# Optimization experiments

Hardware: AMD Instinct MI355X
Metric: run time of the kernel (lower is better)

## Reference

```python
import jax, jax.numpy as jnp
import numpy as np

B, S, D = 4, 1024, 1024
NS = 8            # n_samples
NT = 10           # n_steps
EXP_NOISE = 0.1
STEP = 0.01
TEMP = 1.0
LN_EPS = 1e-5


def _ln(x, g, b):
    m = jnp.mean(x, axis=-1, keepdims=True)
    v = jnp.mean(jnp.square(x - m), axis=-1, keepdims=True)
    return (x - m) * jax.lax.rsqrt(v + LN_EPS) * g + b


def setup_inputs() -> dict:
    key = jax.random.key(0)
    ks = jax.random.split(key, 8)
    sc = 0.02
    return {
        "hidden": jax.random.normal(ks[0], (B, S, D), jnp.float32),
        "W1": jax.random.normal(ks[1], (D, 2 * D), jnp.float32) * sc,
        "b1": jnp.zeros((2 * D,), jnp.float32),
        "ln1_g": jnp.ones((2 * D,), jnp.float32),
        "ln1_b": jnp.zeros((2 * D,), jnp.float32),
        "W2": jax.random.normal(ks[2], (2 * D, D), jnp.float32) * sc,
        "b2": jnp.zeros((D,), jnp.float32),
        "Ew1": jax.random.normal(ks[3], (2 * D, D), jnp.float32) * sc,
        "Eb1": jnp.zeros((D,), jnp.float32),
        "Eln_g": jnp.ones((D,), jnp.float32),
        "Eln_b": jnp.zeros((D,), jnp.float32),
        "Ew2": jax.random.normal(ks[4], (D, D // 2), jnp.float32) * sc,
        "Eb2": jnp.zeros((D // 2,), jnp.float32),
        "Ew3": jax.random.normal(ks[5], (D // 2, 1), jnp.float32) * sc,
        "Eb3": jnp.zeros((1,), jnp.float32),
    }


def reference(hidden, W1, b1, ln1_g, ln1_b, W2, b2,
              Ew1, Eb1, Eln_g, Eln_b, Ew2, Eb2, Ew3, Eb3):
    # context: per-seq mean, identical at every position (keepdim+expand in torch)
    ctx = jnp.mean(hidden, axis=1)                      # [B, D]
    # context_predictor (result is .detach()-ed inside pcn_refine)
    cp = jax.nn.relu(_ln(ctx @ W1 + b1, ln1_g, ln1_b)) @ W2 + b2   # [B, D]
    cp = jax.lax.stop_gradient(cp)

    nkey = jax.random.key(42)
    # n_samples exploration hypotheses: hidden + N(0, exploration_noise)
    expl = jax.random.normal(jax.random.fold_in(nkey, 0), (NS, B, S, D), hidden.dtype)
    hyp = hidden[None] + expl * EXP_NOISE               # [NS, B, S, D]

    cpb = cp[None, :, None, :]                          # broadcast to [NS,B,S,D]

    # PCN refinement: linear pull toward cp + small noise on all but last step
    def step_fn(cur, t):
        cur = cur - STEP * (cur - cpb)
        noise = jax.random.normal(jax.random.fold_in(nkey, t + 1), cur.shape, cur.dtype)
        cur = cur + noise * 0.01 * (t < NT - 1)
        return cur, None

    hyp, _ = jax.lax.scan(step_fn, hyp, jnp.arange(NT))

    # energy_net on concat([latent, context]): split first linear to avoid concat
    Ew1_h, Ew1_c = Ew1[:D], Ew1[D:]
    ce = ctx @ Ew1_c + Eb1                              # context contribution [B, D]
    e = hyp @ Ew1_h + ce[None, :, None, :]              # [NS, B, S, D]
    e = jax.nn.relu(_ln(e, Eln_g, Eln_b))
    e = jax.nn.relu(e @ Ew2 + Eb2)                      # [NS, B, S, D//2]
    e = (e @ Ew3 + Eb3)[..., 0]                         # [NS, B, S]
    energies = jnp.mean(e, axis=2)                      # [NS, B]

    probs = jax.nn.softmax(-energies / TEMP, axis=0)    # [NS, B]
    selected = jnp.einsum('nb,nbsd->bsd', probs, hyp)   # [B, S, D]
    return selected
```

## Files before the change

kernel.cpp:

```cpp
#include <hip/hip_runtime.h>
#include <hip/hip_bf16.h>
#include <hip/hip_fp8.h>
#include <stdint.h>
#include <math.h>


#define NS_ 8
#define B_ 4
#define S_ 1024
#define D_ 1024
#define NROWS (NS_*B_*S_)
#define NELEM (1u<<25)

typedef __attribute__((ext_vector_type(8))) short short8;
typedef __attribute__((ext_vector_type(4))) float f32x4;
typedef long i64;

struct RngParams {
  uint32_t k0[10], k1[10];
  float coef[10];
  float aH, aCP;
};

__host__ __device__ __forceinline__ uint32_t rotl32_(uint32_t x, int r) {
#if defined(__HIP_DEVICE_COMPILE__)
  return __builtin_rotateleft32(x, (uint32_t)r);
#else
  return (x << r) | (x >> (32 - r));
#endif
}

__host__ __device__ __forceinline__ void tf2x32(uint32_t k0, uint32_t k1,
                                                uint32_t x0, uint32_t x1,
                                                uint32_t &o0, uint32_t &o1) {
  uint32_t k2 = k0 ^ k1 ^ 0x1BD11BDAu;
  x0 += k0; x1 += k1;
  x0 += x1; x1 = rotl32_(x1, 13); x1 ^= x0;
  x0 += x1; x1 = rotl32_(x1, 15); x1 ^= x0;
  x0 += x1; x1 = rotl32_(x1, 26); x1 ^= x0;
  x0 += x1; x1 = rotl32_(x1, 6);  x1 ^= x0;
  x0 += k1; x1 += k2 + 1u;
  x0 += x1; x1 = rotl32_(x1, 17); x1 ^= x0;
  x0 += x1; x1 = rotl32_(x1, 29); x1 ^= x0;
  x0 += x1; x1 = rotl32_(x1, 16); x1 ^= x0;
  x0 += x1; x1 = rotl32_(x1, 24); x1 ^= x0;
  x0 += k2; x1 += k0 + 2u;
  x0 += x1; x1 = rotl32_(x1, 13); x1 ^= x0;
  x0 += x1; x1 = rotl32_(x1, 15); x1 ^= x0;
  x0 += x1; x1 = rotl32_(x1, 26); x1 ^= x0;
  x0 += x1; x1 = rotl32_(x1, 6);  x1 ^= x0;
  x0 += k0; x1 += k1 + 3u;
  x0 += x1; x1 = rotl32_(x1, 17); x1 ^= x0;
  x0 += x1; x1 = rotl32_(x1, 29); x1 ^= x0;
  x0 += x1; x1 = rotl32_(x1, 16); x1 ^= x0;
  x0 += x1; x1 = rotl32_(x1, 24); x1 ^= x0;
  x0 += k1; x1 += k2 + 4u;
  x0 += x1; x1 = rotl32_(x1, 13); x1 ^= x0;
  x0 += x1; x1 = rotl32_(x1, 15); x1 ^= x0;
  x0 += x1; x1 = rotl32_(x1, 26); x1 ^= x0;
  x0 += x1; x1 = rotl32_(x1, 6);  x1 ^= x0;
  x0 += k2; x1 += k0 + 5u;
  o0 = x0; o1 = x1;
}

__device__ __forceinline__ float b2n_scaled(uint32_t bits) {
  const float lo = -0.99999994f;
  float f = __uint_as_float((bits >> 9) | 0x3f800000u);
  float x = fmaxf(lo, fmaf(f, 2.0f, lo - 2.0f));
  float t = fmaf(-x, x, 1.0f);
  float l2 = __log2f(t);
  float p;
  if (l2 > -7.2134752f) {
    float v = fmaf(l2, -1.0f, -3.6067376f);
    p = 2.11766e-09f;
    p = fmaf(p, v, 3.73196e-08f);
    p = fmaf(p, v, -5.52622e-07f);
    p = fmaf(p, v, -9.93683e-07f);
    p = fmaf(p, v, 7.13556e-05f);
    p = fmaf(p, v, -5.90466e-04f);
    p = fmaf(p, v, -2.83857e-03f);
    p = fmaf(p, v, 2.41772e-01f);
    p = fmaf(p, v, 2.1233136f);
  } else {
    float s = sqrtf(l2 * -0.69314718f) - 3.0f;
    p = -2.83146e-04f;
    p = fmaf(p, s, 1.42766e-04f);
    p = fmaf(p, s, 1.90826e-03f);
    p = fmaf(p, s, -5.19503e-03f);
    p = fmaf(p, s, 8.11695e-03f);
    p = fmaf(p, s, -1.07799e-02f);
    p = fmaf(p, s, 1.33486e-02f);
    p = fmaf(p, s, 1.41658104f);
    p = fmaf(p, s, 4.00643763f);
  }
  return p * x;
}

__device__ __forceinline__ void noise10x2(const RngParams& P, uint32_t i0,
                                          float& n0, float& n1) {
  float a0 = 0.f, a1 = 0.f;
  #pragma unroll 2
  for (int j = 0; j < 10; ++j) {
    uint32_t w0, w1, v0, v1;
    tf2x32(P.k0[j], P.k1[j], 0u, i0, w0, w1);
    tf2x32(P.k0[j], P.k1[j], 0u, i0 + 1u, v0, v1);
    float c = P.coef[j];
    a0 = fmaf(c, b2n_scaled(w0 ^ w1), a0);
    a1 = fmaf(c, b2n_scaled(v0 ^ v1), a1);
  }
  n0 = a0; n1 = a1;
}

__device__ __forceinline__ float noise10(const RngParams& P, uint32_t i) {
  float acc = 0.f;
  #pragma unroll 2
  for (int j = 0; j < 10; ++j) {
    uint32_t w0, w1;
    tf2x32(P.k0[j], P.k1[j], 0u, i, w0, w1);
    acc = fmaf(P.coef[j], b2n_scaled(w0 ^ w1), acc);
  }
  return acc;
}

__device__ __forceinline__ uint16_t bf16u(float x) {
  __hip_bfloat16 h = __float2bfloat16(x);
  return *(uint16_t*)&h;
}
__device__ __forceinline__ float bf2f(uint32_t u) {
  return __uint_as_float(u << 16);
}
__device__ __forceinline__ uint8_t f2e4m3(float x) {
  __hip_fp8_e4m3 h(x);
  return (uint8_t)h.__x;
}
__device__ __forceinline__ float e4m32f(uint8_t u) {
  __hip_fp8_e4m3 h;
  h.__x = u;
  return (float)h;
}

__device__ void wcvt_body(const float* __restrict__ src, uint16_t* __restrict__ dst,
                          int K, int N, int bx, int by) {
  __shared__ float tile[64][65];
  int n0 = bx * 64, k0 = by * 64;
  int tid = threadIdx.x;
  #pragma unroll
  for (int i = 0; i < 16; ++i) {
    int lin = tid + i * 256;
    int tr = lin >> 6, tc = lin & 63;
    tile[tr][tc] = src[(size_t)(k0 + tr) * N + n0 + tc];
  }
  __syncthreads();
  #pragma unroll
  for (int i = 0; i < 8; ++i) {
    int lin = tid + i * 256;
    int tr = lin >> 5, tc2 = (lin & 31) * 2;
    uint32_t pk = (uint32_t)bf16u(tile[tc2][tr]) | ((uint32_t)bf16u(tile[tc2 + 1][tr]) << 16);
    *(uint32_t*)(&dst[(size_t)(n0 + tr) * K + k0 + tc2]) = pk;
  }
}

__device__ void wcvt8_body(const float* __restrict__ src, uint8_t* __restrict__ dst,
                           int K, int N, int bx, int by) {
  __shared__ float tile[64][65];
  int n0 = bx * 64, k0 = by * 64;
  int tid = threadIdx.x;
  #pragma unroll
  for (int i = 0; i < 16; ++i) {
    int lin = tid + i * 256;
    int tr = lin >> 6, tc = lin & 63;
    tile[tr][tc] = src[(size_t)(k0 + tr) * N + n0 + tc];
  }
  __syncthreads();
  #pragma unroll
  for (int i = 0; i < 8; ++i) {
    int lin = tid + i * 256;
    int tr = lin >> 5, tc2 = (lin & 31) * 2;
    uint16_t pk = (uint16_t)f2e4m3(tile[tc2][tr]) | ((uint16_t)f2e4m3(tile[tc2 + 1][tr]) << 8);
    *(uint16_t*)(&dst[(size_t)(n0 + tr) * K + k0 + tc2]) = pk;
  }
}

__global__ void k_prep(const float* __restrict__ Ew1, const float* __restrict__ Ew2,
                       const float* __restrict__ hidden,
                       uint16_t* __restrict__ WT1, uint8_t* __restrict__ WT2,
                       float* __restrict__ part) {
  int bi = blockIdx.x;
  if (bi < 256) {
    wcvt_body(Ew1, WT1, 1024, 1024, bi & 15, bi >> 4);
  } else if (bi < 384) {
    int j = bi - 256;
    wcvt8_body(Ew2, WT2, 1024, 512, j & 7, j >> 3);
  } else {
    int cb = bi - 384;
    int b = cb >> 6, ch = cb & 63;
    const float* p = hidden + (size_t)b * (S_ * D_) + (size_t)ch * 16 * 1024;
    int tid = threadIdx.x;
    #pragma unroll
    for (int k = 0; k < 4; ++k) {
      int d = tid + k * 256;
      float s = 0.f;
      #pragma unroll
      for (int t = 0; t < 16; ++t) s += p[t * 1024 + d];
      part[(size_t)cb * 1024 + d] = s;
    }
  }
}

__global__ void k_ctxB(const float* __restrict__ part, float* __restrict__ ctx) {
  int idx = blockIdx.x * 256 + threadIdx.x;
  int b = idx >> 10, d = idx & 1023;
  float s = 0.f;
  #pragma unroll 8
  for (int c = 0; c < 64; ++c) s += part[((size_t)(b * 64 + c)) * 1024 + d];
  ctx[idx] = s * (1.0f / 1024.0f);
}

__global__ void k_fc1(const float* __restrict__ ctx, const float* __restrict__ W1,
                      const float* __restrict__ b1, float* __restrict__ t1) {
  __shared__ float red[4][64];
  int b = blockIdx.x >> 5;
  int j0 = (blockIdx.x & 31) * 64;
  int l = threadIdx.x & 63, w = threadIdx.x >> 6;
  int j = j0 + l;
  const float* c = ctx + b * 1024 + w * 256;
  const float* wp = W1 + (size_t)(w * 256) * 2048 + j;
  float s = 0.f;
  #pragma unroll 8
  for (int k = 0; k < 256; ++k) s += c[k] * wp[(size_t)k * 2048];
  red[w][l] = s; __syncthreads();
  if (w == 0)
    t1[b * 2048 + j] = red[0][l] + red[1][l] + red[2][l] + red[3][l] + b1[j];
}

__global__ void k_ln_relu(float* __restrict__ t1, const float* __restrict__ g,
                          const float* __restrict__ bb) {
  __shared__ float red[256];
  int row = blockIdx.x, tid = threadIdx.x;
  float* x = t1 + row * 2048;
  float v[8];
  #pragma unroll
  for (int q = 0; q < 8; ++q) v[q] = x[tid + q * 256];
  float s = 0.f;
  #pragma unroll
  for (int q = 0; q < 8; ++q) s += v[q];
  red[tid] = s; __syncthreads();
  for (int off = 128; off > 0; off >>= 1) { if (tid < off) red[tid] += red[tid + off]; __syncthreads(); }
  float m = red[0] * (1.0f / 2048.0f);
  __syncthreads();
  float s2 = 0.f;
  #pragma unroll
  for (int q = 0; q < 8; ++q) { float d = v[q] - m; s2 += d * d; }
  red[tid] = s2; __syncthreads();
  for (int off = 128; off > 0; off >>= 1) { if (tid < off) red[tid] += red[tid + off]; __syncthreads(); }
  float var = red[0] * (1.0f / 2048.0f);
  float rs = 1.0f / sqrtf(var + 1e-5f);
  #pragma unroll
  for (int q = 0; q < 8; ++q) {
    int j = tid + q * 256;
    float z = (v[q] - m) * rs * g[j] + bb[j];
    x[j] = fmaxf(z, 0.0f);
  }
}

__global__ void k_fc2(const float* __restrict__ t1, const float* __restrict__ W2,
                      const float* __restrict__ b2, const float* __restrict__ ctx,
                      const float* __restrict__ Ew1c, const float* __restrict__ Eb1,
                      float* __restrict__ cp, float* __restrict__ ce) {
  __shared__ float red[4][64];
  int b = blockIdx.x >> 4;
  int j0 = (blockIdx.x & 15) * 64;
  int l = threadIdx.x & 63, w = threadIdx.x >> 6;
  int j = j0 + l;
  float s = 0.f;
  if (blockIdx.y == 0) {
    const float* a = t1 + b * 2048 + w * 512;
    const float* wp = W2 + (size_t)(w * 512) * 1024 + j;
    #pragma unroll 8
    for (int k = 0; k < 512; ++k) s += a[k] * wp[(size_t)k * 1024];
  } else {
    const float* a = ctx + b * 1024 + w * 256;
    const float* wp = Ew1c + (size_t)(w * 256) * 1024 + j;
    #pragma unroll 8
    for (int k = 0; k < 256; ++k) s += a[k] * wp[(size_t)k * 1024];
  }
  red[w][l] = s; __syncthreads();
  if (w == 0) {
    float r = red[0][l] + red[1][l] + red[2][l] + red[3][l];
    if (blockIdx.y == 0) cp[b * 1024 + j] = r + b2[j];
    else                 ce[b * 1024 + j] = r + Eb1[j];
  }
}

__global__ __launch_bounds__(256) void k_noise(
    const float* __restrict__ hidden, const float* __restrict__ cp,
    uint32_t* __restrict__ hypPairs, RngParams P)
{
  uint32_t pe = blockIdx.x * 256u + threadIdx.x;
  uint32_t i0 = pe * 2u;
  float nz0, nz1;
  noise10x2(P, i0, nz0, nz1);
  uint32_t b = (i0 >> 20) & 3u;
  float2 hv = *(const float2*)(hidden + (i0 & 0x3FFFFFu));
  float2 cv = *(const float2*)(cp + ((b << 10) | (i0 & 1023u)));
  float h0 = fmaf(P.aH, hv.x, fmaf(P.aCP, cv.x, nz0));
  float h1 = fmaf(P.aH, hv.y, fmaf(P.aCP, cv.y, nz1));
  hypPairs[pe] = (uint32_t)bf16u(h0) | ((uint32_t)bf16u(h1) << 16);
}

#define ZP8_OF    0
#define GRED2_OF  65536
#define GSTM_OF   (65536 + 2048)
#define GSTR_OF   (65536 + 2048 + 256)
#define GRED_OF   (65536 + 2048 + 512)
#define GSMEM_END (65536 + 2048 + 512 + 1024)

__device__ __forceinline__ int pswz8(int row, int byteInRow) {
  return (row * 1024 + (byteInRow ^ ((row & 7) << 3)));
}

__global__ __launch_bounds__(256, 2) void k_genergy(
    const uint32_t* __restrict__ hypPairs, const float* __restrict__ ce,
    const uint16_t* __restrict__ WT1, const uint8_t* __restrict__ WT2,
    const float* __restrict__ Eln_g, const float* __restrict__ Eln_b,
    const float* __restrict__ Eb2, const float* __restrict__ Ew3,
    float* __restrict__ erows)
{
  __shared__ __align__(16) char smem[GSMEM_END];
  const int tid = threadIdx.x;
  const int lane = tid & 63;
  const int w = tid >> 6;
  const int rl = lane & 15;
  const int kg = lane >> 4;
  const int r0 = blockIdx.x * 64;
  const int bidx = (r0 >> 10) & 3;
  float* red2 = (float*)(smem + GRED2_OF);
  float* rowm = (float*)(smem + GSTM_OF);
  float* rowr = (float*)(smem + GSTR_OF);
  float* red  = (float*)(smem + GRED_OF);

  float s1a[16], s2a[16];
  #pragma unroll
  for (int i = 0; i < 16; ++i) { s1a[i] = 0.f; s2a[i] = 0.f; }
  const uint16_t* Ab = (const uint16_t*)hypPairs + (size_t)(r0 + rl) * 1024 + kg * 8;
  for (int g = 0; g < 4; ++g) {
    f32x4 acc[4][4];
    #pragma unroll
    for (int rt = 0; rt < 4; ++rt)
      #pragma unroll
      for (int j = 0; j < 4; ++j) acc[rt][j] = (f32x4){0.f, 0.f, 0.f, 0.f};
    const uint16_t* b0 = WT1 + (size_t)(g * 256 + w * 64 +  0 + rl) * 1024 + kg * 8;
    const uint16_t* b1p = WT1 + (size_t)(g * 256 + w * 64 + 16 + rl) * 1024 + kg * 8;
    const uint16_t* b2p = WT1 + (size_t)(g * 256 + w * 64 + 32 + rl) * 1024 + kg * 8;
    const uint16_t* b3p = WT1 + (size_t)(g * 256 + w * 64 + 48 + rl) * 1024 + kg * 8;
    #pragma unroll 4
    for (int kt = 0; kt < 32; ++kt) {
      short8 bf0 = *(const short8*)(b0  + kt * 32);
      short8 bf1 = *(const short8*)(b1p + kt * 32);
      short8 bf2 = *(const short8*)(b2p + kt * 32);
      short8 bf3 = *(const short8*)(b3p + kt * 32);
      #pragma unroll
      for (int rt = 0; rt < 4; ++rt) {
        short8 af = *(const short8*)(Ab + (size_t)rt * 16384 + kt * 32);
        acc[rt][0] = __builtin_amdgcn_mfma_f32_16x16x32_bf16(af, bf0, acc[rt][0], 0, 0, 0);
        acc[rt][1] = __builtin_amdgcn_mfma_f32_16x16x32_bf16(af, bf1, acc[rt][1], 0, 0, 0);
        acc[rt][2] = __builtin_amdgcn_mfma_f32_16x16x32_bf16(af, bf2, acc[rt][2], 0, 0, 0);
        acc[rt][3] = __builtin_amdgcn_mfma_f32_16x16x32_bf16(af, bf3, acc[rt][3], 0, 0, 0);
      }
    }
    #pragma unroll
    for (int rt = 0; rt < 4; ++rt)
      #pragma unroll
      for (int j = 0; j < 4; ++j) {
        int C = g * 256 + w * 64 + j * 16 + rl;
        float cev = ce[(bidx << 10) + C];
        #pragma unroll
        for (int i = 0; i < 4; ++i) {
          float y = acc[rt][j][i] + cev;
          int si = rt * 4 + i;
          s1a[si] += y;
          s2a[si] = fmaf(y, y, s2a[si]);
          *(uint8_t*)(smem + ZP8_OF + pswz8(rt * 16 + kg * 4 + i, C)) = f2e4m3(y);
        }
      }
  }
  #pragma unroll
  for (int i = 0; i < 16; ++i) {
    #pragma unroll
    for (int m = 1; m < 16; m <<= 1) {
      s1a[i] += __shfl_xor(s1a[i], m);
      s2a[i] += __shfl_xor(s2a[i], m);
    }
  }
  if (rl == 0) {
    #pragma unroll
    for (int i = 0; i < 16; ++i) {
      int row = (i >> 2) * 16 + kg * 4 + (i & 3);
      red2[(w * 64 + row) * 2 + 0] = s1a[i];
      red2[(w * 64 + row) * 2 + 1] = s2a[i];
    }
  }
  __syncthreads();

  if (tid < 64) {
    float s1 = red2[tid * 2] + red2[(64 + tid) * 2] + red2[(128 + tid) * 2] + red2[(192 + tid) * 2];
    float s2 = red2[tid * 2 + 1] + red2[(64 + tid) * 2 + 1] + red2[(128 + tid) * 2 + 1] + red2[(192 + tid) * 2 + 1];
    float m = s1 * (1.0f / 1024.0f);
    float var = fmaxf(s2 * (1.0f / 1024.0f) - m * m, 0.0f);
    rowm[tid] = m;
    rowr[tid] = 1.0f / sqrtf(var + 1e-5f);
  }
  __syncthreads();

  {
    float4 gg = *(const float4*)(Eln_g + tid * 4);
    float4 bb4 = *(const float4*)(Eln_b + tid * 4);
    #pragma unroll 1
    for (int row = 0; row < 64; ++row) {
      float m = rowm[row], rs = rowr[row];
      uint32_t* zp = (uint32_t*)(smem + ZP8_OF + pswz8(row, tid * 4));
      uint32_t v = *zp;
      float z0 = fmaf((e4m32f((uint8_t)(v      )) - m) * rs, gg.x, bb4.x);
      float z1 = fmaf((e4m32f((uint8_t)(v >>  8)) - m) * rs, gg.y, bb4.y);
      float z2 = fmaf((e4m32f((uint8_t)(v >> 16)) - m) * rs, gg.z, bb4.z);
      float z3 = fmaf((e4m32f((uint8_t)(v >> 24)) - m) * rs, gg.w, bb4.w);
      *zp = (uint32_t)f2e4m3(fmaxf(z0, 0.f)) |
            ((uint32_t)f2e4m3(fmaxf(z1, 0.f)) << 8) |
            ((uint32_t)f2e4m3(fmaxf(z2, 0.f)) << 16) |
            ((uint32_t)f2e4m3(fmaxf(z3, 0.f)) << 24);
    }
  }
  __syncthreads();

  float ep[16];
  #pragma unroll
  for (int i = 0; i < 16; ++i) ep[i] = 0.f;
  for (int g = 0; g < 2; ++g) {
    f32x4 acc[4][4];
    #pragma unroll
    for (int rt = 0; rt < 4; ++rt)
      #pragma unroll
      for (int j = 0; j < 4; ++j) acc[rt][j] = (f32x4){0.f, 0.f, 0.f, 0.f};
    const uint8_t* c0 = WT2 + (size_t)(g * 256 + w * 64 +  0 + rl) * 1024 + kg * 8;
    const uint8_t* c1 = WT2 + (size_t)(g * 256 + w * 64 + 16 + rl) * 1024 + kg * 8;
    const uint8_t* c2 = WT2 + (size_t)(g * 256 + w * 64 + 32 + rl) * 1024 + kg * 8;
    const uint8_t* c3 = WT2 + (size_t)(g * 256 + w * 64 + 48 + rl) * 1024 + kg * 8;
    #pragma unroll 4
    for (int kt = 0; kt < 32; ++kt) {
      i64 bf0 = *(const i64*)(c0 + kt * 32);
      i64 bf1 = *(const i64*)(c1 + kt * 32);
      i64 bf2 = *(const i64*)(c2 + kt * 32);
      i64 bf3 = *(const i64*)(c3 + kt * 32);
      #pragma unroll
      for (int rt = 0; rt < 4; ++rt) {
        i64 af = *(const i64*)(smem + ZP8_OF + pswz8(rt * 16 + rl, kt * 32 + kg * 8));
        acc[rt][0] = __builtin_amdgcn_mfma_f32_16x16x32_fp8_fp8(af, bf0, acc[rt][0], 0, 0, 0);
        acc[rt][1] = __builtin_amdgcn_mfma_f32_16x16x32_fp8_fp8(af, bf1, acc[rt][1], 0, 0, 0);
        acc[rt][2] = __builtin_amdgcn_mfma_f32_16x16x32_fp8_fp8(af, bf2, acc[rt][2], 0, 0, 0);
        acc[rt][3] = __builtin_amdgcn_mfma_f32_16x16x32_fp8_fp8(af, bf3, acc[rt][3], 0, 0, 0);
      }
    }
    #pragma unroll
    for (int rt = 0; rt < 4; ++rt)
      #pragma unroll
      for (int j = 0; j < 4; ++j) {
        int C = g * 256 + w * 64 + j * 16 + rl;
        float eb = Eb2[C], w3 = Ew3[C];
        #pragma unroll
        for (int i = 0; i < 4; ++i)
          ep[rt * 4 + i] = fmaf(fmaxf(acc[rt][j][i] + eb, 0.f), w3, ep[rt * 4 + i]);
      }
  }
  #pragma unroll
  for (int i = 0; i < 16; ++i) {
    #pragma unroll
    for (int m = 1; m < 16; m <<= 1) ep[i] += __shfl_xor(ep[i], m);
  }
  if (rl == 0) {
    #pragma unroll
    for (int i = 0; i < 16; ++i) {
      int row = (i >> 2) * 16 + kg * 4 + (i & 3);
      red[w * 64 + row] = ep[i];
    }
  }
  __syncthreads();
  if (tid < 64)
    erows[r0 + tid] = red[tid] + red[64 + tid] + red[128 + tid] + red[192 + tid];
}

__global__ void k_energy(const float* __restrict__ erows, const float* __restrict__ Eb3,
                         float* __restrict__ energ) {
  __shared__ float red[256];
  int nb = blockIdx.x, tid = threadIdx.x;
  const float* x = erows + nb * 1024;
  float s = x[tid] + x[tid + 256] + x[tid + 512] + x[tid + 768];
  red[tid] = s; __syncthreads();
  for (int off = 128; off > 0; off >>= 1) { if (tid < off) red[tid] += red[tid + off]; __syncthreads(); }
  if (tid == 0) energ[nb] = red[0] * (1.0f / 1024.0f) + Eb3[0];
}

#define FZP_OF    0
#define FRED2_OF  16384
#define FSTM_OF   16896
#define FSTR_OF   16960
#define FRED_OF   17024
#define FAPAN_OF  17280

__device__ __forceinline__ int pswz(int row, int byteInRow) {
  return (row * 2048 + byteInRow) ^ ((row & 7) << 4);
}

__global__ __launch_bounds__(256, 2) void k_fused_small(
    const float* __restrict__ hidden, const float* __restrict__ cp,
    const float* __restrict__ ce,
    const uint16_t* __restrict__ WT1, const uint8_t* __restrict__ WT2,
    const float* __restrict__ Eln_g, const float* __restrict__ Eln_b,
    const float* __restrict__ Eb2, const float* __restrict__ Ew3,
    float* __restrict__ erows, RngParams P)
{
  __shared__ __align__(16) char smem[FAPAN_OF + 32768];
  const int tid = threadIdx.x;
  const int lane = tid & 63;
  const int w = tid >> 6;
  const int rl = lane & 15;
  const int kg = lane >> 4;
  const int r0 = blockIdx.x * 16;
  const int bidx = (r0 >> 10) & 3;
  float* rowm = (float*)(smem + FSTM_OF);
  float* rowr = (float*)(smem + FSTR_OF);
  float* red  = (float*)(smem + FRED_OF);
  float* red2 = (float*)(smem + FRED2_OF);

  for (int q = 0; q < 32; ++q) {
    int p = tid + q * 256;
    int row = p >> 9, c0 = (p & 511) * 2;
    uint32_t i0 = (uint32_t)(r0 + row) * 1024u + (uint32_t)c0;
    float nz0, nz1;
    noise10x2(P, i0, nz0, nz1);
    float2 hv = *(const float2*)(hidden + (i0 & 0x3FFFFFu));
    float2 cv = *(const float2*)(cp + (bidx << 10) + c0);
    float h0 = fmaf(P.aH, hv.x, fmaf(P.aCP, cv.x, nz0));
    float h1 = fmaf(P.aH, hv.y, fmaf(P.aCP, cv.y, nz1));
    uint32_t pk = (uint32_t)bf16u(h0) | ((uint32_t)bf16u(h1) << 16);
    *(uint32_t*)(smem + FAPAN_OF + pswz(row, c0 * 2)) = pk;
  }
  __syncthreads();

  float s1a[4] = {0.f, 0.f, 0.f, 0.f};
  float s2a[4] = {0.f, 0.f, 0.f, 0.f};
  for (int g = 0; g < 4; ++g) {
    f32x4 acc[4] = {};
    const uint16_t* b0 = WT1 + (size_t)(g * 256 + w * 64 +  0 + rl) * 1024 + kg * 8;
    const uint16_t* b1p = WT1 + (size_t)(g * 256 + w * 64 + 16 + rl) * 1024 + kg * 8;
    const uint16_t* b2p = WT1 + (size_t)(g * 256 + w * 64 + 32 + rl) * 1024 + kg * 8;
    const uint16_t* b3p = WT1 + (size_t)(g * 256 + w * 64 + 48 + rl) * 1024 + kg * 8;
    #pragma unroll 8
    for (int kt = 0; kt < 32; ++kt) {
      short8 af = *(const short8*)(smem + FAPAN_OF + pswz(rl, kt * 64 + kg * 16));
      short8 f0 = *(const short8*)(b0  + kt * 32);
      short8 f1 = *(const short8*)(b1p + kt * 32);
      short8 f2 = *(const short8*)(b2p + kt * 32);
      short8 f3 = *(const short8*)(b3p + kt * 32);
      acc[0] = __builtin_amdgcn_mfma_f32_16x16x32_bf16(af, f0, acc[0], 0, 0, 0);
      acc[1] = __builtin_amdgcn_mfma_f32_16x16x32_bf16(af, f1, acc[1], 0, 0, 0);
      acc[2] = __builtin_amdgcn_mfma_f32_16x16x32_bf16(af, f2, acc[2], 0, 0, 0);
      acc[3] = __builtin_amdgcn_mfma_f32_16x16x32_bf16(af, f3, acc[3], 0, 0, 0);
    }
    #pragma unroll
    for (int j = 0; j < 4; ++j) {
      int C = g * 256 + w * 64 + j * 16 + rl;
      float cev = ce[(bidx << 10) + C];
      #pragma unroll
      for (int i = 0; i < 4; ++i) {
        float y = acc[j][i] + cev;
        s1a[i] += y;
        s2a[i] = fmaf(y, y, s2a[i]);
        *(uint8_t*)(smem + FZP_OF + pswz8(kg * 4 + i, C)) = f2e4m3(y);
      }
    }
  }
  #pragma unroll
  for (int i = 0; i < 4; ++i) {
    #pragma unroll
    for (int m = 1; m < 16; m <<= 1) {
      s1a[i] += __shfl_xor(s1a[i], m);
      s2a[i] += __shfl_xor(s2a[i], m);
    }
  }
  if (rl == 0) {
    #pragma unroll
    for (int i = 0; i < 4; ++i) {
      red2[(w * 16 + kg * 4 + i) * 2 + 0] = s1a[i];
      red2[(w * 16 + kg * 4 + i) * 2 + 1] = s2a[i];
    }
  }
  __syncthreads();
  if (tid < 16) {
    float s1 = 0.f, s2 = 0.f;
    #pragma unroll
    for (int wv = 0; wv < 4; ++wv) {
      s1 += red2[(wv * 16 + tid) * 2 + 0];
      s2 += red2[(wv * 16 + tid) * 2 + 1];
    }
    float m = s1 * (1.0f / 1024.0f);
    float var = fmaxf(s2 * (1.0f / 1024.0f) - m * m, 0.0f);
    rowm[tid] = m;
    rowr[tid] = 1.0f / sqrtf(var + 1e-5f);
  }
  __syncthreads();
  {
    float4 gg = *(const float4*)(Eln_g + tid * 4);
    float4 bb4 = *(const float4*)(Eln_b + tid * 4);
    #pragma unroll 1
    for (int row = 0; row < 16; ++row) {
      float m = rowm[row], rs = rowr[row];
      uint32_t* zp = (uint32_t*)(smem + FZP_OF + pswz8(row, tid * 4));
      uint32_t v = *zp;
      float z0 = fmaf((e4m32f((uint8_t)(v      )) - m) * rs, gg.x, bb4.x);
      float z1 = fmaf((e4m32f((uint8_t)(v >>  8)) - m) * rs, gg.y, bb4.y);
      float z2 = fmaf((e4m32f((uint8_t)(v >> 16)) - m) * rs, gg.z, bb4.z);
      float z3 = fmaf((e4m32f((uint8_t)(v >> 24)) - m) * rs, gg.w, bb4.w);
      *zp = (uint32_t)f2e4m3(fmaxf(z0, 0.f)) |
            ((uint32_t)f2e4m3(fmaxf(z1, 0.f)) << 8) |
            ((uint32_t)f2e4m3(fmaxf(z2, 0.f)) << 16) |
            ((uint32_t)f2e4m3(fmaxf(z3, 0.f)) << 24);
    }
  }
  __syncthreads();
  float ep0 = 0.f, ep1 = 0.f, ep2 = 0.f, ep3 = 0.f;
  for (int g = 0; g < 2; ++g) {
    f32x4 acc[4] = {};
    const uint8_t* c0 = WT2 + (size_t)(g * 256 + w * 64 +  0 + rl) * 1024 + kg * 8;
    const uint8_t* c1 = WT2 + (size_t)(g * 256 + w * 64 + 16 + rl) * 1024 + kg * 8;
    const uint8_t* c2 = WT2 + (size_t)(g * 256 + w * 64 + 32 + rl) * 1024 + kg * 8;
    const uint8_t* c3 = WT2 + (size_t)(g * 256 + w * 64 + 48 + rl) * 1024 + kg * 8;
    #pragma unroll 8
    for (int kt = 0; kt < 32; ++kt) {
      i64 af = *(const i64*)(smem + FZP_OF + pswz8(rl, kt * 32 + kg * 8));
      i64 f0 = *(const i64*)(c0 + kt * 32);
      i64 f1 = *(const i64*)(c1 + kt * 32);
      i64 f2 = *(const i64*)(c2 + kt * 32);
      i64 f3 = *(const i64*)(c3 + kt * 32);
      acc[0] = __builtin_amdgcn_mfma_f32_16x16x32_fp8_fp8(af, f0, acc[0], 0, 0, 0);
      acc[1] = __builtin_amdgcn_mfma_f32_16x16x32_fp8_fp8(af, f1, acc[1], 0, 0, 0);
      acc[2] = __builtin_amdgcn_mfma_f32_16x16x32_fp8_fp8(af, f2, acc[2], 0, 0, 0);
      acc[3] = __builtin_amdgcn_mfma_f32_16x16x32_fp8_fp8(af, f3, acc[3], 0, 0, 0);
    }
    #pragma unroll
    for (int j = 0; j < 4; ++j) {
      int C = g * 256 + w * 64 + j * 16 + rl;
      float eb = Eb2[C], w3 = Ew3[C];
      ep0 = fmaf(fmaxf(acc[j][0] + eb, 0.f), w3, ep0);
      ep1 = fmaf(fmaxf(acc[j][1] + eb, 0.f), w3, ep1);
      ep2 = fmaf(fmaxf(acc[j][2] + eb, 0.f), w3, ep2);
      ep3 = fmaf(fmaxf(acc[j][3] + eb, 0.f), w3, ep3);
    }
  }
  #pragma unroll
  for (int m = 1; m < 16; m <<= 1) {
    ep0 += __shfl_xor(ep0, m);
    ep1 += __shfl_xor(ep1, m);
    ep2 += __shfl_xor(ep2, m);
    ep3 += __shfl_xor(ep3, m);
  }
  if (rl == 0) {
    red[w * 16 + kg * 4 + 0] = ep0;
    red[w * 16 + kg * 4 + 1] = ep1;
    red[w * 16 + kg * 4 + 2] = ep2;
    red[w * 16 + kg * 4 + 3] = ep3;
  }
  __syncthreads();
  if (tid < 16)
    erows[r0 + tid] = red[tid] + red[16 + tid] + red[32 + tid] + red[48 + tid];
}

template<bool BIG>
__global__ __launch_bounds__(256) void k_select(
    const float* __restrict__ hidden, const float* __restrict__ cp,
    const float* __restrict__ energ, const uint32_t* __restrict__ hypPairs,
    float* __restrict__ out, RngParams P)
{
  uint32_t pe = blockIdx.x * 256u + threadIdx.x;
  uint32_t i0 = pe * 2u;
  uint32_t b = (i0 >> 20) & 3u;
  float e[8];
  #pragma unroll
  for (int n = 0; n < 8; ++n) e[n] = -energ[n * 4 + b];
  float mx = e[0];
  #pragma unroll
  for (int n = 1; n < 8; ++n) mx = fmaxf(mx, e[n]);
  float p[8]; float s = 0.f;
  #pragma unroll
  for (int n = 0; n < 8; ++n) { p[n] = expf(e[n] - mx); s += p[n]; }
  float inv = 1.0f / s;
  float a0 = 0.f, a1 = 0.f;
  if (BIG) {
    #pragma unroll
    for (int n = 0; n < 8; ++n) {
      uint32_t pk = hypPairs[pe + ((uint32_t)n << 21)];
      a0 = fmaf(p[n], __uint_as_float(pk << 16), a0);
      a1 = fmaf(p[n], __uint_as_float(pk & 0xffff0000u), a1);
    }
    *(float2*)(out + i0) = make_float2(a0 * inv, a1 * inv);
  } else {
    float2 hv = *(const float2*)(hidden + i0);
    float2 cv = *(const float2*)(cp + ((b << 10) | (i0 & 1023u)));
    #pragma unroll
    for (int n = 0; n < 8; ++n) {
      a0 = fmaf(p[n], noise10(P, i0 + ((uint32_t)n << 22)), a0);
      a1 = fmaf(p[n], noise10(P, i0 + 1u + ((uint32_t)n << 22)), a1);
    }
    float o0 = fmaf(P.aH, hv.x, P.aCP * cv.x) + a0 * inv;
    float o1 = fmaf(P.aH, hv.y, P.aCP * cv.y) + a1 * inv;
    *(float2*)(out + i0) = make_float2(o0, o1);
  }
}

extern "C" void kernel_launch(void* const* d_in, const int* in_sizes, int n_in,
                              void* d_out, int out_size, void* d_ws, size_t ws_size,
                              hipStream_t stream) {
  const float* hidden = (const float*)d_in[0];
  const float* W1    = (const float*)d_in[1];
  const float* b1    = (const float*)d_in[2];
  const float* ln1_g = (const float*)d_in[3];
  const float* ln1_b = (const float*)d_in[4];
  const float* W2    = (const float*)d_in[5];
  const float* b2    = (const float*)d_in[6];
  const float* Ew1   = (const float*)d_in[7];
  const float* Eb1   = (const float*)d_in[8];
  const float* Eln_g = (const float*)d_in[9];
  const float* Eln_b = (const float*)d_in[10];
  const float* Ew2   = (const float*)d_in[11];
  const float* Eb2   = (const float*)d_in[12];
  const float* Ew3   = (const float*)d_in[13];
  const float* Eb3   = (const float*)d_in[14];
  float* out = (float*)d_out;

  const size_t HYP_B  = (size_t)NELEM * 2;
  const size_t WT1_B  = 1024ull * 1024 * 2;
  const size_t WT2_B  = 512ull * 1024;
  const size_t PART_B = 256ull * 1024 * 4;
  const size_t SMALL_B = (4096 + 8192 + 4096 + 4096 + 32768 + 32) * 4;
  bool big = ws_size >= HYP_B + WT1_B + WT2_B + PART_B + SMALL_B + 1024;

  char* ws = (char*)d_ws;
  uint32_t* hypPairs = nullptr;
  size_t off = 0;
  if (big) { hypPairs = (uint32_t*)ws; off += HYP_B; }
  uint16_t* WT1 = (uint16_t*)(ws + off); off += WT1_B;
  uint8_t*  WT2 = (uint8_t*)(ws + off);  off += WT2_B;
  float* part  = (float*)(ws + off);     off += PART_B;
  float* ctx   = (float*)(ws + off);
  float* t1    = ctx + 4096;
  float* cp    = t1 + 8192;
  float* ce    = cp + 4096;
  float* erows = ce + 4096;
  float* energ = erows + 32768;

  RngParams P;
  for (uint32_t t = 0; t < 10; ++t) {
    uint32_t o0, o1;
    tf2x32(0u, 42u, 0u, t, o0, o1);
    P.k0[t] = o0; P.k1[t] = o1;
  }
  double a = pow(0.99, 10);
  P.coef[0] = (float)(0.1 * a);
  for (int j = 1; j <= 9; ++j) P.coef[j] = (float)(0.01 * pow(0.99, 10 - j));
  P.aH = (float)a;
  P.aCP = (float)(1.0 - a);

  k_prep<<<640, 256, 0, stream>>>(Ew1, Ew2, hidden, WT1, WT2, part);
  k_ctxB<<<16, 256, 0, stream>>>(part, ctx);
  k_fc1<<<128, 256, 0, stream>>>(ctx, W1, b1, t1);
  k_ln_relu<<<4, 256, 0, stream>>>(t1, ln1_g, ln1_b);
  k_fc2<<<dim3(64, 2), 256, 0, stream>>>(t1, W2, b2, ctx, Ew1 + (size_t)1024 * 1024, Eb1, cp, ce);
  if (big) {
    k_noise<<<65536, 256, 0, stream>>>(hidden, cp, hypPairs, P);
    k_genergy<<<512, 256, 0, stream>>>(hypPairs, ce, WT1, WT2, Eln_g, Eln_b,
                                       Eb2, Ew3, erows);
  } else {
    k_fused_small<<<2048, 256, 0, stream>>>(hidden, cp, ce, WT1, WT2,
                                            Eln_g, Eln_b, Eb2, Ew3, erows, P);
  }
  k_energy<<<32, 256, 0, stream>>>(erows, Eb3, energ);
  if (big)
    k_select<true><<<8192, 256, 0, stream>>>(hidden, cp, energ, hypPairs, out, P);
  else
    k_select<false><<<8192, 256, 0, stream>>>(hidden, cp, energ, nullptr, out, P);
}
```

Baseline: 976.4 us.

## Remove cp dependency from noise pass and fold it into prep kernel

The hypothesis tensor is now built without the context-predictor term, so noise generation no longer waits on the small context MLP chain and runs in the same launch as the weight conversion and context partial sums. The missing aCP*cp term is restored algebraically: its contribution to the first energy linear is added to ce by a new k_ce2 matvec, and it is added back in the final selection because the softmax weights sum to one. This removes a dependency and a separate launch, in exchange for one extra small kernel. The hypotheses are stored in bf16 without the cp offset, which slightly changes rounding.

```diff
diff --git a/kernel.cpp b/kernel.cpp
--- a/kernel.cpp
+++ b/kernel.cpp
@@ -140,57 +140,67 @@
 }
 
 __device__ void wcvt_body(const float* __restrict__ src, uint16_t* __restrict__ dst,
-                          int K, int N, int bx, int by) {
-  __shared__ float tile[64][65];
+                          int K, int N, int bx, int by, float* tile ) {
   int n0 = bx * 64, k0 = by * 64;
   int tid = threadIdx.x;
   #pragma unroll
   for (int i = 0; i < 16; ++i) {
     int lin = tid + i * 256;
     int tr = lin >> 6, tc = lin & 63;
-    tile[tr][tc] = src[(size_t)(k0 + tr) * N + n0 + tc];
+    tile[tr * 65 + tc] = src[(size_t)(k0 + tr) * N + n0 + tc];
   }
   __syncthreads();
   #pragma unroll
   for (int i = 0; i < 8; ++i) {
     int lin = tid + i * 256;
     int tr = lin >> 5, tc2 = (lin & 31) * 2;
-    uint32_t pk = (uint32_t)bf16u(tile[tc2][tr]) | ((uint32_t)bf16u(tile[tc2 + 1][tr]) << 16);
+    uint32_t pk = (uint32_t)bf16u(tile[tc2 * 65 + tr]) | ((uint32_t)bf16u(tile[(tc2 + 1) * 65 + tr]) << 16);
     *(uint32_t*)(&dst[(size_t)(n0 + tr) * K + k0 + tc2]) = pk;
   }
 }
 
 __device__ void wcvt8_body(const float* __restrict__ src, uint8_t* __restrict__ dst,
-                           int K, int N, int bx, int by) {
-  __shared__ float tile[64][65];
+                           int K, int N, int bx, int by, float* tile) {
   int n0 = bx * 64, k0 = by * 64;
   int tid = threadIdx.x;
   #pragma unroll
   for (int i = 0; i < 16; ++i) {
     int lin = tid + i * 256;
     int tr = lin >> 6, tc = lin & 63;
-    tile[tr][tc] = src[(size_t)(k0 + tr) * N + n0 + tc];
+    tile[tr * 65 + tc] = src[(size_t)(k0 + tr) * N + n0 + tc];
   }
   __syncthreads();
   #pragma unroll
   for (int i = 0; i < 8; ++i) {
     int lin = tid + i * 256;
     int tr = lin >> 5, tc2 = (lin & 31) * 2;
-    uint16_t pk = (uint16_t)f2e4m3(tile[tc2][tr]) | ((uint16_t)f2e4m3(tile[tc2 + 1][tr]) << 8);
+    uint16_t pk = (uint16_t)f2e4m3(tile[tc2 * 65 + tr]) | ((uint16_t)f2e4m3(tile[(tc2 + 1) * 65 + tr]) << 8);
     *(uint16_t*)(&dst[(size_t)(n0 + tr) * K + k0 + tc2]) = pk;
   }
 }
 
-__global__ void k_prep(const float* __restrict__ Ew1, const float* __restrict__ Ew2,
-                       const float* __restrict__ hidden,
-                       uint16_t* __restrict__ WT1, uint8_t* __restrict__ WT2,
-                       float* __restrict__ part) {
+__global__ __launch_bounds__(256) void k_mega(
+    const float* __restrict__ Ew1, const float* __restrict__ Ew2,
+    const float* __restrict__ hidden,
+    uint16_t* __restrict__ WT1, uint8_t* __restrict__ WT2,
+    float* __restrict__ part, uint32_t* __restrict__ hypPairs, RngParams P)
+{
+  __shared__ float tile[64 * 65];
   int bi = blockIdx.x;
-  if (bi < 256) {
-    wcvt_body(Ew1, WT1, 1024, 1024, bi & 15, bi >> 4);
+  if (bi >= 640) {
+    uint32_t pe = (uint32_t)(bi - 640) * 256u + threadIdx.x;
+    uint32_t i0 = pe * 2u;
+    float nz0, nz1;
+    noise10x2(P, i0, nz0, nz1);
+    float2 hv = *(const float2*)(hidden + (i0 & 0x3FFFFFu));
+    float h0 = fmaf(P.aH, hv.x, nz0);
+    float h1 = fmaf(P.aH, hv.y, nz1);
+    hypPairs[pe] = (uint32_t)bf16u(h0) | ((uint32_t)bf16u(h1) << 16);
+  } else if (bi < 256) {
+    wcvt_body(Ew1, WT1, 1024, 1024, bi & 15, bi >> 4, tile);
   } else if (bi < 384) {
     int j = bi - 256;
-    wcvt8_body(Ew2, WT2, 1024, 512, j & 7, j >> 3);
+    wcvt8_body(Ew2, WT2, 1024, 512, j & 7, j >> 3, tile);
   } else {
     int cb = bi - 384;
     int b = cb >> 6, ch = cb & 63;
@@ -292,20 +302,21 @@
   }
 }
 
-__global__ __launch_bounds__(256) void k_noise(
-    const float* __restrict__ hidden, const float* __restrict__ cp,
-    uint32_t* __restrict__ hypPairs, RngParams P)
-{
-  uint32_t pe = blockIdx.x * 256u + threadIdx.x;
-  uint32_t i0 = pe * 2u;
-  float nz0, nz1;
-  noise10x2(P, i0, nz0, nz1);
-  uint32_t b = (i0 >> 20) & 3u;
-  float2 hv = *(const float2*)(hidden + (i0 & 0x3FFFFFu));
-  float2 cv = *(const float2*)(cp + ((b << 10) | (i0 & 1023u)));
-  float h0 = fmaf(P.aH, hv.x, fmaf(P.aCP, cv.x, nz0));
-  float h1 = fmaf(P.aH, hv.y, fmaf(P.aCP, cv.y, nz1));
-  hypPairs[pe] = (uint32_t)bf16u(h0) | ((uint32_t)bf16u(h1) << 16);
+__global__ void k_ce2(const float* __restrict__ cp, const float* __restrict__ Ew1,
+                      float aCP, float* __restrict__ ce) {
+  __shared__ float red[4][64];
+  int b = blockIdx.x >> 4;
+  int j0 = (blockIdx.x & 15) * 64;
+  int l = threadIdx.x & 63, w = threadIdx.x >> 6;
+  int j = j0 + l;
+  const float* a = cp + b * 1024 + w * 256;
+  const float* wp = Ew1 + (size_t)(w * 256) * 1024 + j;
+  float s = 0.f;
+  #pragma unroll 8
+  for (int k = 0; k < 256; ++k) s += a[k] * wp[(size_t)k * 1024];
+  red[w][l] = s; __syncthreads();
+  if (w == 0)
+    ce[b * 1024 + j] += aCP * (red[0][l] + red[1][l] + red[2][l] + red[3][l]);
 }
 
 #define ZP8_OF    0
@@ -701,7 +712,10 @@
       a0 = fmaf(p[n], __uint_as_float(pk << 16), a0);
       a1 = fmaf(p[n], __uint_as_float(pk & 0xffff0000u), a1);
     }
-    *(float2*)(out + i0) = make_float2(a0 * inv, a1 * inv);
+    float2 cv = *(const float2*)(cp + ((b << 10) | (i0 & 1023u)));
+    float o0 = fmaf(a0, inv, P.aCP * cv.x);
+    float o1 = fmaf(a1, inv, P.aCP * cv.y);
+    *(float2*)(out + i0) = make_float2(o0, o1);
   } else {
     float2 hv = *(const float2*)(hidden + i0);
     float2 cv = *(const float2*)(cp + ((b << 10) | (i0 & 1023u)));
@@ -769,22 +783,28 @@
   P.aH = (float)a;
   P.aCP = (float)(1.0 - a);
 
-  k_prep<<<640, 256, 0, stream>>>(Ew1, Ew2, hidden, WT1, WT2, part);
-  k_ctxB<<<16, 256, 0, stream>>>(part, ctx);
-  k_fc1<<<128, 256, 0, stream>>>(ctx, W1, b1, t1);
-  k_ln_relu<<<4, 256, 0, stream>>>(t1, ln1_g, ln1_b);
-  k_fc2<<<dim3(64, 2), 256, 0, stream>>>(t1, W2, b2, ctx, Ew1 + (size_t)1024 * 1024, Eb1, cp, ce);
   if (big) {
-    k_noise<<<65536, 256, 0, stream>>>(hidden, cp, hypPairs, P);
+    k_mega<<<640 + 65536, 256, 0, stream>>>(Ew1, Ew2, hidden, WT1, WT2, part,
+                                            hypPairs, P);
+    k_ctxB<<<16, 256, 0, stream>>>(part, ctx);
+    k_fc1<<<128, 256, 0, stream>>>(ctx, W1, b1, t1);
+    k_ln_relu<<<4, 256, 0, stream>>>(t1, ln1_g, ln1_b);
+    k_fc2<<<dim3(64, 2), 256, 0, stream>>>(t1, W2, b2, ctx, Ew1 + (size_t)1024 * 1024, Eb1, cp, ce);
+    k_ce2<<<64, 256, 0, stream>>>(cp, Ew1, P.aCP, ce);
     k_genergy<<<512, 256, 0, stream>>>(hypPairs, ce, WT1, WT2, Eln_g, Eln_b,
                                        Eb2, Ew3, erows);
+    k_energy<<<32, 256, 0, stream>>>(erows, Eb3, energ);
+    k_select<true><<<8192, 256, 0, stream>>>(hidden, cp, energ, hypPairs, out, P);
   } else {
+    k_mega<<<640, 256, 0, stream>>>(Ew1, Ew2, hidden, WT1, WT2, part,
+                                    (uint32_t*)ws, P);
+    k_ctxB<<<16, 256, 0, stream>>>(part, ctx);
+    k_fc1<<<128, 256, 0, stream>>>(ctx, W1, b1, t1);
+    k_ln_relu<<<4, 256, 0, stream>>>(t1, ln1_g, ln1_b);
+    k_fc2<<<dim3(64, 2), 256, 0, stream>>>(t1, W2, b2, ctx, Ew1 + (size_t)1024 * 1024, Eb1, cp, ce);
     k_fused_small<<<2048, 256, 0, stream>>>(hidden, cp, ce, WT1, WT2,
                                             Eln_g, Eln_b, Eb2, Ew3, erows, P);
-  }
-  k_energy<<<32, 256, 0, stream>>>(erows, Eb3, energ);
-  if (big)
-    k_select<true><<<8192, 256, 0, stream>>>(hidden, cp, energ, hypPairs, out, P);
-  else
+    k_energy<<<32, 256, 0, stream>>>(erows, Eb3, energ);
     k_select<false><<<8192, 256, 0, stream>>>(hidden, cp, energ, nullptr, out, P);
-}
+  }
+}
```

Result: slower. 1.011 ms (+3.5%).
